# Optimization experiments

Measured on AMD Instinct MI355X. Metric: run time of the kernel, lower is better.

## Reference

```python
import jax, jax.numpy as jnp
import numpy as np

NPOINT = 1024
NSAMPLE = 32


def _fps(xyz, npoint):
    # farthest point sampling; xyz: (B, N, 3) -> idx (B, npoint) int32
    B, N, _ = xyz.shape

    def step(carry, _):
        dist, far = carry
        centroid = jnp.take_along_axis(xyz, far[:, None, None], axis=1)  # (B,1,3)
        d = jnp.sum((xyz - centroid) ** 2, axis=-1)  # (B,N)
        dist = jnp.minimum(dist, d)
        nxt = jnp.argmax(dist, axis=1).astype(jnp.int32)
        return (dist, nxt), far

    init = (jnp.full((B, N), 1e10, xyz.dtype), jnp.zeros((B,), jnp.int32))
    _, idx = jax.lax.scan(step, init, None, length=npoint)
    return idx.T  # (B, npoint)


def _forward(xyz, features, afa_w1, afa_b1, afa_w2, afa_b2, afa_ww, afa_bw,
             mlp_w1, mlp_b1, mlp_w2, mlp_b2, mlp_w3, mlp_b3):
    B, N, _ = xyz.shape
    M = NSAMPLE
    # --- furthest point sampling + gather new_xyz ---
    fps_idx = _fps(xyz, NPOINT)                                   # (B, Np)
    new_xyz = jnp.take_along_axis(xyz, fps_idx[..., None], axis=1)  # (B, Np, 3)
    # --- kNN grouping (QueryAndGroup with use_xyz) ---
    sqd = (jnp.sum(new_xyz ** 2, -1)[..., None]
           + jnp.sum(xyz ** 2, -1)[:, None, :]
           - 2.0 * jnp.einsum('bpd,bnd->bpn', new_xyz, xyz))       # (B, Np, N)
    _, knn = jax.lax.top_k(-sqd, M)                               # (B, Np, M)
    gather = jax.vmap(lambda a, i: a[i])
    gxyz = gather(xyz, knn) - new_xyz[:, :, None, :]              # (B, Np, M, 3)
    gfeat = gather(features.transpose(0, 2, 1), knn)              # (B, Np, M, Cin)
    x = jnp.concatenate([gxyz, gfeat], axis=-1).transpose(0, 3, 1, 2)  # (B, C, Np, M)
    # --- AFA: pairwise diff + eye self term ---
    eye = jnp.eye(M, dtype=x.dtype)
    pair = x[..., :, None] - x[..., None, :] + x[..., :, None] * eye  # (B, C, Np, M, M)
    conv5 = lambda w, b, t: jnp.einsum('oc,bcnij->bonij', w, t) + b[None, :, None, None, None]
    h = jax.nn.relu(conv5(afa_w1, afa_b1, pair))
    h = jax.nn.relu(conv5(afa_w2, afa_b2, h))
    wgt = conv5(afa_ww, afa_bw, h)                                 # (B, C, Np, M, M)
    afa = jnp.sum(pair * wgt, axis=-1)                             # (B, C, Np, M)
    nf = x + afa
    # --- shared MLP (1x1 convs, relu, no bn) + max pool over M ---
    conv4 = lambda w, b, t: jnp.einsum('oc,bcnm->bonm', w, t) + b[None, :, None, None]
    h = jax.nn.relu(conv4(mlp_w1, mlp_b1, nf))
    h = jax.nn.relu(conv4(mlp_w2, mlp_b2, h))
    h = jax.nn.relu(conv4(mlp_w3, mlp_b3, h))
    out = jnp.max(h, axis=-1)                                      # (B, 128, Np)
    return new_xyz, out


def setup_inputs() -> dict:
    key = jax.random.key(0)
    ks = jax.random.split(key, 10)
    B, N, Cin = 2, 4096, 32
    C = Cin + 3  # use_xyz adds 3 -> 35

    def w(k, o, i):
        return (jax.random.normal(k, (o, i), jnp.float32) / np.float32(np.sqrt(i)))

    return {
        'xyz': jax.random.uniform(ks[0], (B, N, 3), jnp.float32),
        'features': jax.random.normal(ks[1], (B, Cin, N), jnp.float32),
        'afa_w1': w(ks[2], 16, C), 'afa_b1': jnp.zeros((16,), jnp.float32),
        'afa_w2': w(ks[3], 16, 16), 'afa_b2': jnp.zeros((16,), jnp.float32),
        'afa_ww': w(ks[4], C, 16), 'afa_bw': jnp.zeros((C,), jnp.float32),
        'mlp_w1': w(ks[5], 64, C), 'mlp_b1': jnp.zeros((64,), jnp.float32),
        'mlp_w2': w(ks[6], 64, 64), 'mlp_b2': jnp.zeros((64,), jnp.float32),
        'mlp_w3': w(ks[7], 128, 64), 'mlp_b3': jnp.zeros((128,), jnp.float32),
    }


def reference(xyz, features, afa_w1, afa_b1, afa_w2, afa_b2, afa_ww, afa_bw,
              mlp_w1, mlp_b1, mlp_w2, mlp_b2, mlp_w3, mlp_b3):
    return _forward(xyz, features, afa_w1, afa_b1, afa_w2, afa_b2, afa_ww, afa_bw,
                    mlp_w1, mlp_b1, mlp_w2, mlp_b2, mlp_w3, mlp_b3)
```

## Files before the change

### kernel.cpp

```cpp
#include <hip/hip_runtime.h>

#define BB 2
#define NN 4096
#define NP 1024
#define MM 32
#define CC 35
#define CIN 32

typedef float f2 __attribute__((ext_vector_type(2)));

#define KEY_DPP(CTRL) do { \
    int _lo = (int)(unsigned)key, _hi = (int)(unsigned)(key >> 32); \
    int _olo = __builtin_amdgcn_mov_dpp(_lo, CTRL, 0xF, 0xF, true); \
    int _ohi = __builtin_amdgcn_mov_dpp(_hi, CTRL, 0xF, 0xF, true); \
    unsigned long long _ok = ((unsigned long long)(unsigned)_ohi << 32) | (unsigned)_olo; \
    if (_ok > key) key = _ok; \
} while (0)

__launch_bounds__(256)
__global__ void fps_prep_kernel(const float* __restrict__ xyz, float* __restrict__ newxyz_out,
                                const float* __restrict__ w1, const float* __restrict__ w2,
                                const float* __restrict__ w3,
                                float* __restrict__ w1p, float* __restrict__ w2p,
                                float* __restrict__ w3p)
{
#pragma clang fp contract(off)
    const int t = threadIdx.x;

    if (blockIdx.x >= BB) {
        int g = (blockIdx.x - BB) * 256 + t;
        int stride = 8 * 256;
        for (int i = g; i < 9 * 64 * 4; i += stride) {
            int c4 = i >> 8, o = (i >> 2) & 63, cl = i & 3;
            int c = 4 * c4 + cl;
            w1p[i] = (c < CC) ? w1[o * CC + c] : 0.0f;
        }
        for (int i = g; i < 16 * 64 * 4; i += stride) {
            int c4 = i >> 8, o = (i >> 2) & 63, cl = i & 3;
            w2p[i] = w2[o * 64 + 4 * c4 + cl];
        }
        for (int i = g; i < 16 * 128 * 4; i += stride) {
            int c4 = i >> 9, o = (i >> 2) & 127, cl = i & 3;
            w3p[i] = w3[o * 64 + 4 * c4 + cl];
        }
        return;
    }

    const int b = blockIdx.x;
    const float* xb = xyz + b * NN * 3;

    __shared__ float4 pc[NN];
    __shared__ float nxs[NP * 3];
    __shared__ unsigned long long red[2][16];

    f2 px[8], py[8], pz[8], dist[8];
#pragma unroll
    for (int k = 0; k < 16; ++k) {
        int n = t + 256 * k;
        float x = xb[n * 3 + 0];
        float y = xb[n * 3 + 1];
        float z = xb[n * 3 + 2];
        px[k >> 1][k & 1] = x;
        py[k >> 1][k & 1] = y;
        pz[k >> 1][k & 1] = z;
        dist[k >> 1][k & 1] = 1e10f;
        pc[n] = make_float4(x, y, z, 0.0f);
    }
    __syncthreads();

    int far = 0;
    for (int s = 0; s < NP; ++s) {
        float4 c = pc[far];
        if (t == 0) {
            nxs[s * 3 + 0] = c.x;
            nxs[s * 3 + 1] = c.y;
            nxs[s * 3 + 2] = c.z;
        }
        const f2 cx = { c.x, c.x }, cy = { c.y, c.y }, cz = { c.z, c.z };

        float bv = -1.0f; int bi = 0;
#pragma unroll
        for (int j = 0; j < 8; ++j) {
            f2 dx = px[j] - cx, dy = py[j] - cy, dz = pz[j] - cz;
            f2 d = (dx * dx + dy * dy) + dz * dz;
            f2 dd = __builtin_elementwise_min(dist[j], d);
            dist[j] = dd;
            if (dd.x > bv) { bv = dd.x; bi = t + 256 * (2 * j); }
            if (dd.y > bv) { bv = dd.y; bi = t + 256 * (2 * j + 1); }
        }

        unsigned long long key =
            ((unsigned long long)(unsigned)__float_as_int(bv) << 32)
            | (unsigned)(0xFFFFFFFFu - (unsigned)bi);

        KEY_DPP(0xB1);
        KEY_DPP(0x4E);
        KEY_DPP(0x141);
        KEY_DPP(0x140);

        const int buf = s & 1;
        if ((t & 15) == 0) red[buf][t >> 4] = key;
        __syncthreads();

        key = red[buf][t & 15];
        KEY_DPP(0xB1);
        KEY_DPP(0x4E);
        KEY_DPP(0x141);
        KEY_DPP(0x140);
        far = (int)(0xFFFFFFFFu - (unsigned)key);
    }

    __syncthreads();
#pragma unroll
    for (int j = 0; j < 12; ++j) {
        int i = t + 256 * j;
        newxyz_out[b * NP * 3 + i] = nxs[i];
    }
}

__launch_bounds__(256)
__global__ void knnafa_kernel(const float* __restrict__ xyz, const float* __restrict__ feat,
                              const float* __restrict__ newxyz,
                              const float* __restrict__ aw1, const float* __restrict__ ab1,
                              const float* __restrict__ aw2, const float* __restrict__ ab2,
                              const float* __restrict__ aww, const float* __restrict__ abw,
                              const float* __restrict__ w1p, const float* __restrict__ b1,
                              const float* __restrict__ w2p, const float* __restrict__ b2,
                              const float* __restrict__ w3p, const float* __restrict__ b3,
                              float* __restrict__ out)
{
    const int bp = blockIdx.x;
    const int b = bp >> 10, p = bp & 1023;
    const int t = threadIdx.x;

    union Smem {
        struct {
            unsigned kxs[NN];
            int hist[256];
            int wsum[4];
            unsigned long long blist[512];
        } k;
        struct {
            float xs_t[MM][36];
            float u[MM][20];
            float nfs[CC + 1][MM];
            float h1s[64][36];
            float h2s[64][36];
            float pmax[128][2];
        } a;
    };
    __shared__ Smem S;
    __shared__ int idxs[MM];
    __shared__ int scal[4];

    {
#pragma clang fp contract(off)
        const float* xb = xyz + b * NN * 3;
        const float qx = newxyz[bp * 3 + 0];
        const float qy = newxyz[bp * 3 + 1];
        const float qz = newxyz[bp * 3 + 2];
        const float qn = (qx * qx + qy * qy) + qz * qz;

        S.k.hist[t] = 0;
        if (t < 4) scal[t] = 0;
        __syncthreads();

#pragma unroll
        for (int k = 0; k < 16; ++k) {
            int n = t + 256 * k;
            float x = xb[n * 3 + 0], y = xb[n * 3 + 1], z = xb[n * 3 + 2];
            float xn = (x * x + y * y) + z * z;
            float dt = (qx * x + qy * y) + qz * z;
            float d = (qn + xn) - 2.0f * dt;
            unsigned bits = __float_as_uint(d);
            unsigned kx = bits ^ ((unsigned)((int)bits >> 31) | 0x80000000u);
            S.k.kxs[n] = kx;
            atomicAdd(&S.k.hist[kx >> 24], 1);
        }
        __syncthreads();

        {
            int c = S.k.hist[t];
            int incl = c;
            const int lane = t & 63, w = t >> 6;
#pragma unroll
            for (int off = 1; off < 64; off <<= 1) {
                int o = __shfl_up(incl, off);
                if (lane >= off) incl += o;
            }
            if (lane == 63) S.k.wsum[w] = incl;
            __syncthreads();
            int base = 0;
            for (int ww = 0; ww < 4; ++ww) if (ww < w) base += S.k.wsum[ww];
            int excl = base + incl - c;
            if (excl < MM && MM <= excl + c) { scal[0] = t; scal[1] = excl; }
        }
        __syncthreads();

        const int B = scal[0];
        const int cntBelow = scal[1];
        const unsigned bstart = (unsigned)B << 24;

#pragma unroll
        for (int k = 0; k < 16; ++k) {
            int n = t + 256 * k;
            unsigned kx = S.k.kxs[n];
            if (kx < bstart) {
                int pos = atomicAdd(&scal[3], 1);
                idxs[pos] = n;
            } else if ((kx >> 24) == (unsigned)B) {
                int pos = atomicAdd(&scal[2], 1);
                if (pos < 512) S.k.blist[pos] = ((unsigned long long)kx << 32) | (unsigned)n;
            }
        }
        __syncthreads();

        const int nB = scal[2];
        const int k2 = MM - cntBelow;

        if (nB <= 512) {
            for (int m = t; m < nB; m += 256) {
                unsigned long long my = S.k.blist[m];
                int rank = 0;
                for (int q = 0; q < nB; ++q) rank += (S.k.blist[q] < my) ? 1 : 0;
                if (rank < k2)
                    idxs[cntBelow + rank] = (int)(my & 0xFFFFFFFFu);
            }
        } else {
            for (int r = 0; r < MM; ++r) {
                unsigned bvk = 0xFFFFFFFFu; int bi = NN;
#pragma unroll
                for (int k = 0; k < 16; ++k) {
                    int n = t + 256 * k;
                    unsigned v = S.k.kxs[n];
                    if (v < bvk) { bvk = v; bi = n; }
                }
#pragma unroll
                for (int off = 1; off < 64; off <<= 1) {
                    unsigned ov = __shfl_xor(bvk, off);
                    int   oi = __shfl_xor(bi, off);
                    if (ov < bvk || (ov == bvk && oi < bi)) { bvk = ov; bi = oi; }
                }
                if ((t & 63) == 0) { S.k.hist[t >> 6] = (int)bvk; S.k.wsum[t >> 6] = bi; }
                __syncthreads();
                unsigned fv = (unsigned)S.k.hist[0]; int fi = S.k.wsum[0];
#pragma unroll
                for (int w = 1; w < 4; ++w) {
                    unsigned ov = (unsigned)S.k.hist[w]; int oi = S.k.wsum[w];
                    if (ov < fv || (ov == fv && oi < fi)) { fv = ov; fi = oi; }
                }
                if (t == 0) { idxs[r] = fi; S.k.kxs[fi] = 0xFFFFFFFFu; }
                __syncthreads();
            }
        }
    }
    __syncthreads();

    {
        const int m = t & 31, c0 = t >> 5;
        const int id = idxs[m] & (NN - 1);
        for (int c = c0; c < CC; c += 8) {
            float v;
            if (c < 3) v = xyz[(b * NN + id) * 3 + c] - newxyz[bp * 3 + c];
            else       v = feat[(b * CIN + (c - 3)) * NN + id];
            S.a.xs_t[m][c] = v;
        }
        if (c0 == 0) S.a.xs_t[m][35] = 0.0f;
    }
    __syncthreads();

    const int i = t >> 3, jg = t & 7;

    float xi[36];
    {
        const float4* xp = (const float4*)&S.a.xs_t[i][0];
#pragma unroll
        for (int q = 0; q < 9; ++q) {
            float4 v = xp[q];
            xi[4 * q] = v.x; xi[4 * q + 1] = v.y; xi[4 * q + 2] = v.z; xi[4 * q + 3] = v.w;
        }
    }

#pragma unroll
    for (int oo = 0; oo < 2; ++oo) {
        const int o = 2 * jg + oo;
        float acc = 0.0f;
#pragma unroll
        for (int c = 0; c < CC; ++c) acc += aw1[o * CC + c] * xi[c];
        S.a.u[i][o] = acc;
    }
    __syncthreads();

    float ui[16];
    {
        const float4* up = (const float4*)&S.a.u[i][0];
#pragma unroll
        for (int q = 0; q < 4; ++q) {
            float4 v = up[q];
            ui[4 * q] = v.x; ui[4 * q + 1] = v.y; ui[4 * q + 2] = v.z; ui[4 * q + 3] = v.w;
        }
    }

    float afa[CC];
#pragma unroll
    for (int c = 0; c < CC; ++c) afa[c] = 0.0f;

#pragma unroll
    for (int jk = 0; jk < 4; ++jk) {
        const int j = jg + 8 * jk;
        const bool diag = (i == j);

        float uj[16];
        {
            const float4* up = (const float4*)&S.a.u[j][0];
#pragma unroll
            for (int q = 0; q < 4; ++q) {
                float4 v = up[q];
                uj[4 * q] = v.x; uj[4 * q + 1] = v.y; uj[4 * q + 2] = v.z; uj[4 * q + 3] = v.w;
            }
        }

        float h1[16];
#pragma unroll
        for (int o = 0; o < 16; ++o) {
            float sv = ui[o] - uj[o];
            if (diag) sv += ui[o];
            h1[o] = fmaxf(sv + ab1[o], 0.0f);
        }

        float xj[36];
        {
            const float4* xp = (const float4*)&S.a.xs_t[j][0];
#pragma unroll
            for (int q = 0; q < 9; ++q) {
                float4 v = xp[q];
                xj[4 * q] = v.x; xj[4 * q + 1] = v.y; xj[4 * q + 2] = v.z; xj[4 * q + 3] = v.w;
            }
        }

        float h2[16];
#pragma unroll
        for (int o = 0; o < 16; ++o) {
            float acc = ab2[o];
#pragma unroll
            for (int c = 0; c < 16; ++c) acc += aw2[o * 16 + c] * h1[c];
            h2[o] = fmaxf(acc, 0.0f);
        }

#pragma unroll
        for (int c = 0; c < CC; ++c) {
            float acc = abw[c];
#pragma unroll
            for (int k = 0; k < 16; ++k) acc += aww[c * 16 + k] * h2[k];
            float pc_ = xi[c] - xj[c];
            if (diag) pc_ += xi[c];
            afa[c] += pc_ * acc;
        }
    }

#pragma unroll
    for (int c = 0; c < CC; ++c) {
        float v = afa[c];
        v += __shfl_xor(v, 1);
        v += __shfl_xor(v, 2);
        v += __shfl_xor(v, 4);
        if (jg == 0) S.a.nfs[c][i] = xi[c] + v;
    }
    if (jg == 0) S.a.nfs[35][i] = 0.0f;
    __syncthreads();

    {
        const int o = t & 63, ib = (t >> 6) << 3;
        float acc[8];
        float bb = b1[o];
#pragma unroll
        for (int k = 0; k < 8; ++k) acc[k] = bb;
        const float4* wp = (const float4*)w1p;
#pragma unroll
        for (int c4 = 0; c4 < 9; ++c4) {
            float4 w = wp[c4 * 64 + o];
#pragma unroll
            for (int cl = 0; cl < 4; ++cl) {
                const int c = 4 * c4 + cl;
                float wc = ((const float*)&w)[cl];
                const float4* np4 = (const float4*)&S.a.nfs[c][ib];
                float4 n0 = np4[0], n1 = np4[1];
                acc[0] += wc * n0.x; acc[1] += wc * n0.y; acc[2] += wc * n0.z; acc[3] += wc * n0.w;
                acc[4] += wc * n1.x; acc[5] += wc * n1.y; acc[6] += wc * n1.z; acc[7] += wc * n1.w;
            }
        }
        float4 r0 = { fmaxf(acc[0], 0.0f), fmaxf(acc[1], 0.0f), fmaxf(acc[2], 0.0f), fmaxf(acc[3], 0.0f) };
        float4 r1 = { fmaxf(acc[4], 0.0f), fmaxf(acc[5], 0.0f), fmaxf(acc[6], 0.0f), fmaxf(acc[7], 0.0f) };
        *(float4*)&S.a.h1s[o][ib]     = r0;
        *(float4*)&S.a.h1s[o][ib + 4] = r1;
    }
    __syncthreads();

    {
        const int o = t & 63, ib = (t >> 6) << 3;
        float acc[8];
        float bb = b2[o];
#pragma unroll
        for (int k = 0; k < 8; ++k) acc[k] = bb;
        const float4* wp = (const float4*)w2p;
#pragma unroll
        for (int c4 = 0; c4 < 16; ++c4) {
            float4 w = wp[c4 * 64 + o];
#pragma unroll
            for (int cl = 0; cl < 4; ++cl) {
                const int c = 4 * c4 + cl;
                float wc = ((const float*)&w)[cl];
                const float4* hp4 = (const float4*)&S.a.h1s[c][ib];
                float4 h0 = hp4[0], h1v = hp4[1];
                acc[0] += wc * h0.x; acc[1] += wc * h0.y; acc[2] += wc * h0.z; acc[3] += wc * h0.w;
                acc[4] += wc * h1v.x; acc[5] += wc * h1v.y; acc[6] += wc * h1v.z; acc[7] += wc * h1v.w;
            }
        }
        float4 r0 = { fmaxf(acc[0], 0.0f), fmaxf(acc[1], 0.0f), fmaxf(acc[2], 0.0f), fmaxf(acc[3], 0.0f) };
        float4 r1 = { fmaxf(acc[4], 0.0f), fmaxf(acc[5], 0.0f), fmaxf(acc[6], 0.0f), fmaxf(acc[7], 0.0f) };
        *(float4*)&S.a.h2s[o][ib]     = r0;
        *(float4*)&S.a.h2s[o][ib + 4] = r1;
    }
    __syncthreads();

    {
        const int o = t & 127, ib = (t >> 7) << 4;
        float acc[16];
        float bb = b3[o];
#pragma unroll
        for (int k = 0; k < 16; ++k) acc[k] = bb;
        const float4* wp = (const float4*)w3p;
#pragma unroll
        for (int c4 = 0; c4 < 16; ++c4) {
            float4 w = wp[c4 * 128 + o];
#pragma unroll
            for (int cl = 0; cl < 4; ++cl) {
                const int c = 4 * c4 + cl;
                float wc = ((const float*)&w)[cl];
                const float4* hp4 = (const float4*)&S.a.h2s[c][ib];
                float4 h0 = hp4[0], h1v = hp4[1], h2v = hp4[2], h3v = hp4[3];
                acc[0]  += wc * h0.x;  acc[1]  += wc * h0.y;  acc[2]  += wc * h0.z;  acc[3]  += wc * h0.w;
                acc[4]  += wc * h1v.x; acc[5]  += wc * h1v.y; acc[6]  += wc * h1v.z; acc[7]  += wc * h1v.w;
                acc[8]  += wc * h2v.x; acc[9]  += wc * h2v.y; acc[10] += wc * h2v.z; acc[11] += wc * h2v.w;
                acc[12] += wc * h3v.x; acc[13] += wc * h3v.y; acc[14] += wc * h3v.z; acc[15] += wc * h3v.w;
            }
        }
        float mx = -1e30f;
#pragma unroll
        for (int k = 0; k < 16; ++k) mx = fmaxf(mx, fmaxf(acc[k], 0.0f));
        S.a.pmax[o][t >> 7] = mx;
    }
    __syncthreads();

    if (t < 128) {
        float v = fmaxf(S.a.pmax[t][0], S.a.pmax[t][1]);
        out[(b * 128 + t) * NP + p] = v;
    }
}

extern "C" void kernel_launch(void* const* d_in, const int* in_sizes, int n_in,
                              void* d_out, int out_size, void* d_ws, size_t ws_size,
                              hipStream_t stream)
{
    const float* xyz  = (const float*)d_in[0];
    const float* feat = (const float*)d_in[1];
    const float* aw1  = (const float*)d_in[2];
    const float* ab1  = (const float*)d_in[3];
    const float* aw2  = (const float*)d_in[4];
    const float* ab2  = (const float*)d_in[5];
    const float* aww  = (const float*)d_in[6];
    const float* abw  = (const float*)d_in[7];
    const float* mw1  = (const float*)d_in[8];
    const float* mb1  = (const float*)d_in[9];
    const float* mw2  = (const float*)d_in[10];
    const float* mb2  = (const float*)d_in[11];
    const float* mw3  = (const float*)d_in[12];
    const float* mb3  = (const float*)d_in[13];

    float* out    = (float*)d_out;
    float* newxyz = out;
    float* out2   = out + BB * NP * 3;

    float* w1p = (float*)d_ws;
    float* w2p = w1p + 9 * 64 * 4;
    float* w3p = w2p + 16 * 64 * 4;

    fps_prep_kernel<<<dim3(BB + 8), dim3(256), 0, stream>>>(xyz, newxyz,
                                                            mw1, mw2, mw3, w1p, w2p, w3p);
    knnafa_kernel<<<dim3(BB * NP), dim3(256), 0, stream>>>(
        xyz, feat, newxyz,
        aw1, ab1, aw2, ab2, aww, abw,
        w1p, mb1, w2p, mb2, w3p, mb3, out2);
}
```

Baseline: 715.6 us.

## Fuse FPS and kNN/AFA into a persistent kernel with progress-flag overlap

Merges the sequential farthest-point-sampling kernel and the per-point kNN/AFA/MLP kernel into one persistent kernel. Two blocks run FPS and publish sampled centroids plus a progress counter every 16 steps. The remaining worker blocks spin on that counter and process points as soon as their centroid is ready. This overlaps the long serial FPS chain with the grouping and MLP work. The cost is spin-wait polling, the risk of deadlock if the FPS blocks are not co-resident, and fewer worker blocks (a 512-block grid) looping over 2048 points.

Result: slower. 785.1 us (+9.7%).

```diff
diff --git a/kernel.cpp b/kernel.cpp
--- a/kernel.cpp
+++ b/kernel.cpp
@@ -6,6 +6,7 @@
 #define MM 32
 #define CC 35
 #define CIN 32
+#define WGRID 512
 
 typedef float f2 __attribute__((ext_vector_type(2)));
 
@@ -17,444 +18,465 @@
     if (_ok > key) key = _ok; \
 } while (0)
 
-__launch_bounds__(256)
-__global__ void fps_prep_kernel(const float* __restrict__ xyz, float* __restrict__ newxyz_out,
-                                const float* __restrict__ w1, const float* __restrict__ w2,
-                                const float* __restrict__ w3,
-                                float* __restrict__ w1p, float* __restrict__ w2p,
-                                float* __restrict__ w3p)
+__global__ void prep_kernel(const float* __restrict__ w1, const float* __restrict__ w2,
+                            const float* __restrict__ w3,
+                            float* __restrict__ w1p, float* __restrict__ w2p,
+                            float* __restrict__ w3p, int* __restrict__ progress)
 {
+    int g = blockIdx.x * 256 + threadIdx.x;
+    int stride = gridDim.x * 256;
+    if (g < 2) progress[g] = 0;
+    for (int i = g; i < 9 * 64 * 4; i += stride) {
+        int c4 = i >> 8, o = (i >> 2) & 63, cl = i & 3;
+        int c = 4 * c4 + cl;
+        w1p[i] = (c < CC) ? w1[o * CC + c] : 0.0f;
+    }
+    for (int i = g; i < 16 * 64 * 4; i += stride) {
+        int c4 = i >> 8, o = (i >> 2) & 63, cl = i & 3;
+        w2p[i] = w2[o * 64 + 4 * c4 + cl];
+    }
+    for (int i = g; i < 16 * 128 * 4; i += stride) {
+        int c4 = i >> 9, o = (i >> 2) & 127, cl = i & 3;
+        w3p[i] = w3[o * 64 + 4 * c4 + cl];
+    }
+}
+
+union MegaSmem {
+    struct {
+        float4 pc[NN];
+        unsigned long long red[2][16];
+    } f;
+    struct {
+        union {
+            struct {
+                unsigned kxs[NN];
+                int hist[256];
+                int wsum[4];
+                unsigned long long blist[512];
+            } k;
+            struct {
+                float xs_t[MM][36];
+                float u[MM][20];
+                float nfs[CC + 1][MM];
+                float h1s[64][36];
+                float h2s[64][36];
+                float pmax[128][2];
+            } a;
+        };
+        int idxs[MM];
+        int scal[4];
+        float qs[3];
+    } w;
+};
+
+__launch_bounds__(256, 2)
+__global__ void mega_kernel(const float* __restrict__ xyz, const float* __restrict__ feat,
+                            float* __restrict__ newxyz,
+                            const float* __restrict__ aw1, const float* __restrict__ ab1,
+                            const float* __restrict__ aw2, const float* __restrict__ ab2,
+                            const float* __restrict__ aww, const float* __restrict__ abw,
+                            const float* __restrict__ w1p, const float* __restrict__ b1,
+                            const float* __restrict__ w2p, const float* __restrict__ b2,
+                            const float* __restrict__ w3p, const float* __restrict__ b3,
+                            float* __restrict__ out, int* __restrict__ progress)
+{
+    __shared__ MegaSmem S;
+    const int t = threadIdx.x;
+
+    if (blockIdx.x < BB) {
 #pragma clang fp contract(off)
-    const int t = threadIdx.x;
-
-    if (blockIdx.x >= BB) {
-        int g = (blockIdx.x - BB) * 256 + t;
-        int stride = 8 * 256;
-        for (int i = g; i < 9 * 64 * 4; i += stride) {
-            int c4 = i >> 8, o = (i >> 2) & 63, cl = i & 3;
-            int c = 4 * c4 + cl;
-            w1p[i] = (c < CC) ? w1[o * CC + c] : 0.0f;
-        }
-        for (int i = g; i < 16 * 64 * 4; i += stride) {
-            int c4 = i >> 8, o = (i >> 2) & 63, cl = i & 3;
-            w2p[i] = w2[o * 64 + 4 * c4 + cl];
-        }
-        for (int i = g; i < 16 * 128 * 4; i += stride) {
-            int c4 = i >> 9, o = (i >> 2) & 127, cl = i & 3;
-            w3p[i] = w3[o * 64 + 4 * c4 + cl];
+        const int b = blockIdx.x;
+        const float* xb = xyz + b * NN * 3;
+
+        f2 px[8], py[8], pz[8], dist[8];
+#pragma unroll
+        for (int k = 0; k < 16; ++k) {
+            int n = t + 256 * k;
+            float x = xb[n * 3 + 0];
+            float y = xb[n * 3 + 1];
+            float z = xb[n * 3 + 2];
+            px[k >> 1][k & 1] = x;
+            py[k >> 1][k & 1] = y;
+            pz[k >> 1][k & 1] = z;
+            dist[k >> 1][k & 1] = 1e10f;
+            S.f.pc[n] = make_float4(x, y, z, 0.0f);
+        }
+        __syncthreads();
+
+        int far = 0;
+        for (int s = 0; s < NP; ++s) {
+            float4 c = S.f.pc[far];
+            if (t == 0) {
+                __hip_atomic_store(&newxyz[(b * NP + s) * 3 + 0], c.x,
+                                   __ATOMIC_RELAXED, __HIP_MEMORY_SCOPE_AGENT);
+                __hip_atomic_store(&newxyz[(b * NP + s) * 3 + 1], c.y,
+                                   __ATOMIC_RELAXED, __HIP_MEMORY_SCOPE_AGENT);
+                __hip_atomic_store(&newxyz[(b * NP + s) * 3 + 2], c.z,
+                                   __ATOMIC_RELAXED, __HIP_MEMORY_SCOPE_AGENT);
+            }
+            const f2 cx = { c.x, c.x }, cy = { c.y, c.y }, cz = { c.z, c.z };
+
+            float bv = -1.0f; int bi = 0;
+#pragma unroll
+            for (int j = 0; j < 8; ++j) {
+                f2 dx = px[j] - cx, dy = py[j] - cy, dz = pz[j] - cz;
+                f2 d = (dx * dx + dy * dy) + dz * dz;
+                f2 dd = __builtin_elementwise_min(dist[j], d);
+                dist[j] = dd;
+                if (dd.x > bv) { bv = dd.x; bi = t + 256 * (2 * j); }
+                if (dd.y > bv) { bv = dd.y; bi = t + 256 * (2 * j + 1); }
+            }
+
+            unsigned long long key =
+                ((unsigned long long)(unsigned)__float_as_int(bv) << 32)
+                | (unsigned)(0xFFFFFFFFu - (unsigned)bi);
+
+            KEY_DPP(0xB1);
+            KEY_DPP(0x4E);
+            KEY_DPP(0x141);
+            KEY_DPP(0x140);
+
+            const int buf = s & 1;
+            if ((t & 15) == 0) S.f.red[buf][t >> 4] = key;
+            __syncthreads();
+
+            key = S.f.red[buf][t & 15];
+            KEY_DPP(0xB1);
+            KEY_DPP(0x4E);
+            KEY_DPP(0x141);
+            KEY_DPP(0x140);
+            far = (int)(0xFFFFFFFFu - (unsigned)key);
+
+            if (t == 0 && (s & 15) == 15)
+                __hip_atomic_store(&progress[b], s + 1, __ATOMIC_RELEASE,
+                                   __HIP_MEMORY_SCOPE_AGENT);
         }
         return;
     }
 
-    const int b = blockIdx.x;
-    const float* xb = xyz + b * NN * 3;
-
-    __shared__ float4 pc[NN];
-    __shared__ float nxs[NP * 3];
-    __shared__ unsigned long long red[2][16];
-
-    f2 px[8], py[8], pz[8], dist[8];
-#pragma unroll
-    for (int k = 0; k < 16; ++k) {
-        int n = t + 256 * k;
-        float x = xb[n * 3 + 0];
-        float y = xb[n * 3 + 1];
-        float z = xb[n * 3 + 2];
-        px[k >> 1][k & 1] = x;
-        py[k >> 1][k & 1] = y;
-        pz[k >> 1][k & 1] = z;
-        dist[k >> 1][k & 1] = 1e10f;
-        pc[n] = make_float4(x, y, z, 0.0f);
-    }
-    __syncthreads();
-
-    int far = 0;
-    for (int s = 0; s < NP; ++s) {
-        float4 c = pc[far];
+    for (int pair = blockIdx.x - BB; pair < BB * NP; pair += WGRID - BB) {
+        const int p = pair >> 1, b = pair & 1;
+        const int bp = b * NP + p;
+
         if (t == 0) {
-            nxs[s * 3 + 0] = c.x;
-            nxs[s * 3 + 1] = c.y;
-            nxs[s * 3 + 2] = c.z;
-        }
-        const f2 cx = { c.x, c.x }, cy = { c.y, c.y }, cz = { c.z, c.z };
-
-        float bv = -1.0f; int bi = 0;
-#pragma unroll
-        for (int j = 0; j < 8; ++j) {
-            f2 dx = px[j] - cx, dy = py[j] - cy, dz = pz[j] - cz;
-            f2 d = (dx * dx + dy * dy) + dz * dz;
-            f2 dd = __builtin_elementwise_min(dist[j], d);
-            dist[j] = dd;
-            if (dd.x > bv) { bv = dd.x; bi = t + 256 * (2 * j); }
-            if (dd.y > bv) { bv = dd.y; bi = t + 256 * (2 * j + 1); }
-        }
-
-        unsigned long long key =
-            ((unsigned long long)(unsigned)__float_as_int(bv) << 32)
-            | (unsigned)(0xFFFFFFFFu - (unsigned)bi);
-
-        KEY_DPP(0xB1);
-        KEY_DPP(0x4E);
-        KEY_DPP(0x141);
-        KEY_DPP(0x140);
-
-        const int buf = s & 1;
-        if ((t & 15) == 0) red[buf][t >> 4] = key;
-        __syncthreads();
-
-        key = red[buf][t & 15];
-        KEY_DPP(0xB1);
-        KEY_DPP(0x4E);
-        KEY_DPP(0x141);
-        KEY_DPP(0x140);
-        far = (int)(0xFFFFFFFFu - (unsigned)key);
-    }
-
-    __syncthreads();
-#pragma unroll
-    for (int j = 0; j < 12; ++j) {
-        int i = t + 256 * j;
-        newxyz_out[b * NP * 3 + i] = nxs[i];
-    }
-}
-
-__launch_bounds__(256)
-__global__ void knnafa_kernel(const float* __restrict__ xyz, const float* __restrict__ feat,
-                              const float* __restrict__ newxyz,
-                              const float* __restrict__ aw1, const float* __restrict__ ab1,
-                              const float* __restrict__ aw2, const float* __restrict__ ab2,
-                              const float* __restrict__ aww, const float* __restrict__ abw,
-                              const float* __restrict__ w1p, const float* __restrict__ b1,
-                              const float* __restrict__ w2p, const float* __restrict__ b2,
-                              const float* __restrict__ w3p, const float* __restrict__ b3,
-                              float* __restrict__ out)
-{
-    const int bp = blockIdx.x;
-    const int b = bp >> 10, p = bp & 1023;
-    const int t = threadIdx.x;
-
-    union Smem {
-        struct {
-            unsigned kxs[NN];
-            int hist[256];
-            int wsum[4];
-            unsigned long long blist[512];
-        } k;
-        struct {
-            float xs_t[MM][36];
-            float u[MM][20];
-            float nfs[CC + 1][MM];
-            float h1s[64][36];
-            float h2s[64][36];
-            float pmax[128][2];
-        } a;
-    };
-    __shared__ Smem S;
-    __shared__ int idxs[MM];
-    __shared__ int scal[4];
-
-    {
+            while (__hip_atomic_load(&progress[b], __ATOMIC_RELAXED,
+                                     __HIP_MEMORY_SCOPE_AGENT) <= p)
+                __builtin_amdgcn_s_sleep(32);
+            (void)__hip_atomic_load(&progress[b], __ATOMIC_ACQUIRE,
+                                    __HIP_MEMORY_SCOPE_AGENT);
+            S.w.qs[0] = __hip_atomic_load(&newxyz[bp * 3 + 0], __ATOMIC_RELAXED,
+                                          __HIP_MEMORY_SCOPE_AGENT);
+            S.w.qs[1] = __hip_atomic_load(&newxyz[bp * 3 + 1], __ATOMIC_RELAXED,
+                                          __HIP_MEMORY_SCOPE_AGENT);
+            S.w.qs[2] = __hip_atomic_load(&newxyz[bp * 3 + 2], __ATOMIC_RELAXED,
+                                          __HIP_MEMORY_SCOPE_AGENT);
+        }
+        __syncthreads();
+
+        {
 #pragma clang fp contract(off)
-        const float* xb = xyz + b * NN * 3;
-        const float qx = newxyz[bp * 3 + 0];
-        const float qy = newxyz[bp * 3 + 1];
-        const float qz = newxyz[bp * 3 + 2];
-        const float qn = (qx * qx + qy * qy) + qz * qz;
-
-        S.k.hist[t] = 0;
-        if (t < 4) scal[t] = 0;
-        __syncthreads();
-
-#pragma unroll
-        for (int k = 0; k < 16; ++k) {
-            int n = t + 256 * k;
-            float x = xb[n * 3 + 0], y = xb[n * 3 + 1], z = xb[n * 3 + 2];
-            float xn = (x * x + y * y) + z * z;
-            float dt = (qx * x + qy * y) + qz * z;
-            float d = (qn + xn) - 2.0f * dt;
-            unsigned bits = __float_as_uint(d);
-            unsigned kx = bits ^ ((unsigned)((int)bits >> 31) | 0x80000000u);
-            S.k.kxs[n] = kx;
-            atomicAdd(&S.k.hist[kx >> 24], 1);
-        }
-        __syncthreads();
-
-        {
-            int c = S.k.hist[t];
-            int incl = c;
-            const int lane = t & 63, w = t >> 6;
-#pragma unroll
-            for (int off = 1; off < 64; off <<= 1) {
-                int o = __shfl_up(incl, off);
-                if (lane >= off) incl += o;
-            }
-            if (lane == 63) S.k.wsum[w] = incl;
+            const float* xb = xyz + b * NN * 3;
+            const float qx = S.w.qs[0];
+            const float qy = S.w.qs[1];
+            const float qz = S.w.qs[2];
+            const float qn = (qx * qx + qy * qy) + qz * qz;
+
+            S.w.k.hist[t] = 0;
+            if (t < 4) S.w.scal[t] = 0;
             __syncthreads();
-            int base = 0;
-            for (int ww = 0; ww < 4; ++ww) if (ww < w) base += S.k.wsum[ww];
-            int excl = base + incl - c;
-            if (excl < MM && MM <= excl + c) { scal[0] = t; scal[1] = excl; }
-        }
-        __syncthreads();
-
-        const int B = scal[0];
-        const int cntBelow = scal[1];
-        const unsigned bstart = (unsigned)B << 24;
-
-#pragma unroll
-        for (int k = 0; k < 16; ++k) {
-            int n = t + 256 * k;
-            unsigned kx = S.k.kxs[n];
-            if (kx < bstart) {
-                int pos = atomicAdd(&scal[3], 1);
-                idxs[pos] = n;
-            } else if ((kx >> 24) == (unsigned)B) {
-                int pos = atomicAdd(&scal[2], 1);
-                if (pos < 512) S.k.blist[pos] = ((unsigned long long)kx << 32) | (unsigned)n;
-            }
-        }
-        __syncthreads();
-
-        const int nB = scal[2];
-        const int k2 = MM - cntBelow;
-
-        if (nB <= 512) {
-            for (int m = t; m < nB; m += 256) {
-                unsigned long long my = S.k.blist[m];
-                int rank = 0;
-                for (int q = 0; q < nB; ++q) rank += (S.k.blist[q] < my) ? 1 : 0;
-                if (rank < k2)
-                    idxs[cntBelow + rank] = (int)(my & 0xFFFFFFFFu);
-            }
-        } else {
-            for (int r = 0; r < MM; ++r) {
-                unsigned bvk = 0xFFFFFFFFu; int bi = NN;
-#pragma unroll
-                for (int k = 0; k < 16; ++k) {
-                    int n = t + 256 * k;
-                    unsigned v = S.k.kxs[n];
-                    if (v < bvk) { bvk = v; bi = n; }
-                }
+
+#pragma unroll
+            for (int k = 0; k < 16; ++k) {
+                int n = t + 256 * k;
+                float x = xb[n * 3 + 0], y = xb[n * 3 + 1], z = xb[n * 3 + 2];
+                float xn = (x * x + y * y) + z * z;
+                float dt = (qx * x + qy * y) + qz * z;
+                float d = (qn + xn) - 2.0f * dt;
+                unsigned bits = __float_as_uint(d);
+                unsigned kx = bits ^ ((unsigned)((int)bits >> 31) | 0x80000000u);
+                S.w.k.kxs[n] = kx;
+                atomicAdd(&S.w.k.hist[kx >> 24], 1);
+            }
+            __syncthreads();
+
+            {
+                int c = S.w.k.hist[t];
+                int incl = c;
+                const int lane = t & 63, w = t >> 6;
 #pragma unroll
                 for (int off = 1; off < 64; off <<= 1) {
-                    unsigned ov = __shfl_xor(bvk, off);
-                    int   oi = __shfl_xor(bi, off);
-                    if (ov < bvk || (ov == bvk && oi < bi)) { bvk = ov; bi = oi; }
-                }
-                if ((t & 63) == 0) { S.k.hist[t >> 6] = (int)bvk; S.k.wsum[t >> 6] = bi; }
+                    int o = __shfl_up(incl, off);
+                    if (lane >= off) incl += o;
+                }
+                if (lane == 63) S.w.k.wsum[w] = incl;
                 __syncthreads();
-                unsigned fv = (unsigned)S.k.hist[0]; int fi = S.k.wsum[0];
-#pragma unroll
-                for (int w = 1; w < 4; ++w) {
-                    unsigned ov = (unsigned)S.k.hist[w]; int oi = S.k.wsum[w];
-                    if (ov < fv || (ov == fv && oi < fi)) { fv = ov; fi = oi; }
-                }
-                if (t == 0) { idxs[r] = fi; S.k.kxs[fi] = 0xFFFFFFFFu; }
-                __syncthreads();
-            }
-        }
-    }
-    __syncthreads();
-
-    {
-        const int m = t & 31, c0 = t >> 5;
-        const int id = idxs[m] & (NN - 1);
-        for (int c = c0; c < CC; c += 8) {
-            float v;
-            if (c < 3) v = xyz[(b * NN + id) * 3 + c] - newxyz[bp * 3 + c];
-            else       v = feat[(b * CIN + (c - 3)) * NN + id];
-            S.a.xs_t[m][c] = v;
-        }
-        if (c0 == 0) S.a.xs_t[m][35] = 0.0f;
-    }
-    __syncthreads();
-
-    const int i = t >> 3, jg = t & 7;
-
-    float xi[36];
-    {
-        const float4* xp = (const float4*)&S.a.xs_t[i][0];
-#pragma unroll
-        for (int q = 0; q < 9; ++q) {
-            float4 v = xp[q];
-            xi[4 * q] = v.x; xi[4 * q + 1] = v.y; xi[4 * q + 2] = v.z; xi[4 * q + 3] = v.w;
-        }
-    }
-
-#pragma unroll
-    for (int oo = 0; oo < 2; ++oo) {
-        const int o = 2 * jg + oo;
-        float acc = 0.0f;
-#pragma unroll
-        for (int c = 0; c < CC; ++c) acc += aw1[o * CC + c] * xi[c];
-        S.a.u[i][o] = acc;
-    }
-    __syncthreads();
-
-    float ui[16];
-    {
-        const float4* up = (const float4*)&S.a.u[i][0];
-#pragma unroll
-        for (int q = 0; q < 4; ++q) {
-            float4 v = up[q];
-            ui[4 * q] = v.x; ui[4 * q + 1] = v.y; ui[4 * q + 2] = v.z; ui[4 * q + 3] = v.w;
-        }
-    }
-
-    float afa[CC];
-#pragma unroll
-    for (int c = 0; c < CC; ++c) afa[c] = 0.0f;
-
-#pragma unroll
-    for (int jk = 0; jk < 4; ++jk) {
-        const int j = jg + 8 * jk;
-        const bool diag = (i == j);
-
-        float uj[16];
-        {
-            const float4* up = (const float4*)&S.a.u[j][0];
+                int base = 0;
+                for (int ww = 0; ww < 4; ++ww) if (ww < w) base += S.w.k.wsum[ww];
+                int excl = base + incl - c;
+                if (excl < MM && MM <= excl + c) { S.w.scal[0] = t; S.w.scal[1] = excl; }
+            }
+            __syncthreads();
+
+            const int B = S.w.scal[0];
+            const int cntBelow = S.w.scal[1];
+            const unsigned bstart = (unsigned)B << 24;
+
+#pragma unroll
+            for (int k = 0; k < 16; ++k) {
+                int n = t + 256 * k;
+                unsigned kx = S.w.k.kxs[n];
+                if (kx < bstart) {
+                    int pos = atomicAdd(&S.w.scal[3], 1);
+                    S.w.idxs[pos] = n;
+                } else if ((kx >> 24) == (unsigned)B) {
+                    int pos = atomicAdd(&S.w.scal[2], 1);
+                    if (pos < 512) S.w.k.blist[pos] = ((unsigned long long)kx << 32) | (unsigned)n;
+                }
+            }
+            __syncthreads();
+
+            const int nB = S.w.scal[2];
+            const int k2 = MM - cntBelow;
+
+            if (nB <= 512) {
+                for (int m = t; m < nB; m += 256) {
+                    unsigned long long my = S.w.k.blist[m];
+                    int rank = 0;
+                    for (int q = 0; q < nB; ++q) rank += (S.w.k.blist[q] < my) ? 1 : 0;
+                    if (rank < k2)
+                        S.w.idxs[cntBelow + rank] = (int)(my & 0xFFFFFFFFu);
+                }
+            } else {
+                for (int r = 0; r < MM; ++r) {
+                    unsigned bvk = 0xFFFFFFFFu; int bi = NN;
+#pragma unroll
+                    for (int k = 0; k < 16; ++k) {
+                        int n = t + 256 * k;
+                        unsigned v = S.w.k.kxs[n];
+                        if (v < bvk) { bvk = v; bi = n; }
+                    }
+#pragma unroll
+                    for (int off = 1; off < 64; off <<= 1) {
+                        unsigned ov = __shfl_xor(bvk, off);
+                        int   oi = __shfl_xor(bi, off);
+                        if (ov < bvk || (ov == bvk && oi < bi)) { bvk = ov; bi = oi; }
+                    }
+                    if ((t & 63) == 0) { S.w.k.hist[t >> 6] = (int)bvk; S.w.k.wsum[t >> 6] = bi; }
+                    __syncthreads();
+                    unsigned fv = (unsigned)S.w.k.hist[0]; int fi = S.w.k.wsum[0];
+#pragma unroll
+                    for (int w = 1; w < 4; ++w) {
+                        unsigned ov = (unsigned)S.w.k.hist[w]; int oi = S.w.k.wsum[w];
+                        if (ov < fv || (ov == fv && oi < fi)) { fv = ov; fi = oi; }
+                    }
+                    if (t == 0) { S.w.idxs[r] = fi; S.w.k.kxs[fi] = 0xFFFFFFFFu; }
+                    __syncthreads();
+                }
+            }
+        }
+        __syncthreads();
+
+        {
+            const int m = t & 31, c0 = t >> 5;
+            const int id = S.w.idxs[m] & (NN - 1);
+            for (int c = c0; c < CC; c += 8) {
+                float v;
+                if (c < 3) v = xyz[(b * NN + id) * 3 + c] - S.w.qs[c];
+                else       v = feat[(b * CIN + (c - 3)) * NN + id];
+                S.w.a.xs_t[m][c] = v;
+            }
+            if (c0 == 0) S.w.a.xs_t[m][35] = 0.0f;
+        }
+        __syncthreads();
+
+        const int i = t >> 3, jg = t & 7;
+
+        float xi[36];
+        {
+            const float4* xp = (const float4*)&S.w.a.xs_t[i][0];
+#pragma unroll
+            for (int q = 0; q < 9; ++q) {
+                float4 v = xp[q];
+                xi[4 * q] = v.x; xi[4 * q + 1] = v.y; xi[4 * q + 2] = v.z; xi[4 * q + 3] = v.w;
+            }
+        }
+
+#pragma unroll
+        for (int oo = 0; oo < 2; ++oo) {
+            const int o = 2 * jg + oo;
+            float acc = 0.0f;
+#pragma unroll
+            for (int c = 0; c < CC; ++c) acc += aw1[o * CC + c] * xi[c];
+            S.w.a.u[i][o] = acc;
+        }
+        __syncthreads();
+
+        float ui[16];
+        {
+            const float4* up = (const float4*)&S.w.a.u[i][0];
 #pragma unroll
             for (int q = 0; q < 4; ++q) {
                 float4 v = up[q];
-                uj[4 * q] = v.x; uj[4 * q + 1] = v.y; uj[4 * q + 2] = v.z; uj[4 * q + 3] = v.w;
-            }
-        }
-
-        float h1[16];
-#pragma unroll
-        for (int o = 0; o < 16; ++o) {
-            float sv = ui[o] - uj[o];
-            if (diag) sv += ui[o];
-            h1[o] = fmaxf(sv + ab1[o], 0.0f);
-        }
-
-        float xj[36];
-        {
-            const float4* xp = (const float4*)&S.a.xs_t[j][0];
-#pragma unroll
-            for (int q = 0; q < 9; ++q) {
-                float4 v = xp[q];
-                xj[4 * q] = v.x; xj[4 * q + 1] = v.y; xj[4 * q + 2] = v.z; xj[4 * q + 3] = v.w;
-            }
-        }
-
-        float h2[16];
-#pragma unroll
-        for (int o = 0; o < 16; ++o) {
-            float acc = ab2[o];
-#pragma unroll
-            for (int c = 0; c < 16; ++c) acc += aw2[o * 16 + c] * h1[c];
-            h2[o] = fmaxf(acc, 0.0f);
+                ui[4 * q] = v.x; ui[4 * q + 1] = v.y; ui[4 * q + 2] = v.z; ui[4 * q + 3] = v.w;
+            }
+        }
+
+        float afa[CC];
+#pragma unroll
+        for (int c = 0; c < CC; ++c) afa[c] = 0.0f;
+
+#pragma unroll
+        for (int jk = 0; jk < 4; ++jk) {
+            const int j = jg + 8 * jk;
+            const bool diag = (i == j);
+
+            float uj[16];
+            {
+                const float4* up = (const float4*)&S.w.a.u[j][0];
+#pragma unroll
+                for (int q = 0; q < 4; ++q) {
+                    float4 v = up[q];
+                    uj[4 * q] = v.x; uj[4 * q + 1] = v.y; uj[4 * q + 2] = v.z; uj[4 * q + 3] = v.w;
+                }
+            }
+
+            float h1[16];
+#pragma unroll
+            for (int o = 0; o < 16; ++o) {
+                float sv = ui[o] - uj[o];
+                if (diag) sv += ui[o];
+                h1[o] = fmaxf(sv + ab1[o], 0.0f);
+            }
+
+            float xj[36];
+            {
+                const float4* xp = (const float4*)&S.w.a.xs_t[j][0];
+#pragma unroll
+                for (int q = 0; q < 9; ++q) {
+                    float4 v = xp[q];
+                    xj[4 * q] = v.x; xj[4 * q + 1] = v.y; xj[4 * q + 2] = v.z; xj[4 * q + 3] = v.w;
+                }
+            }
+
+            float h2[16];
+#pragma unroll
+            for (int o = 0; o < 16; ++o) {
+                float acc = ab2[o];
+#pragma unroll
+                for (int c = 0; c < 16; ++c) acc += aw2[o * 16 + c] * h1[c];
+                h2[o] = fmaxf(acc, 0.0f);
+            }
+
+#pragma unroll
+            for (int c = 0; c < CC; ++c) {
+                float acc = abw[c];
+#pragma unroll
+                for (int k = 0; k < 16; ++k) acc += aww[c * 16 + k] * h2[k];
+                float pc_ = xi[c] - xj[c];
+                if (diag) pc_ += xi[c];
+                afa[c] += pc_ * acc;
+            }
         }
 
 #pragma unroll
         for (int c = 0; c < CC; ++c) {
-            float acc = abw[c];
-#pragma unroll
-            for (int k = 0; k < 16; ++k) acc += aww[c * 16 + k] * h2[k];
-            float pc_ = xi[c] - xj[c];
-            if (diag) pc_ += xi[c];
-            afa[c] += pc_ * acc;
-        }
-    }
-
-#pragma unroll
-    for (int c = 0; c < CC; ++c) {
-        float v = afa[c];
-        v += __shfl_xor(v, 1);
-        v += __shfl_xor(v, 2);
-        v += __shfl_xor(v, 4);
-        if (jg == 0) S.a.nfs[c][i] = xi[c] + v;
-    }
-    if (jg == 0) S.a.nfs[35][i] = 0.0f;
-    __syncthreads();
-
-    {
-        const int o = t & 63, ib = (t >> 6) << 3;
-        float acc[8];
-        float bb = b1[o];
-#pragma unroll
-        for (int k = 0; k < 8; ++k) acc[k] = bb;
-        const float4* wp = (const float4*)w1p;
-#pragma unroll
-        for (int c4 = 0; c4 < 9; ++c4) {
-            float4 w = wp[c4 * 64 + o];
-#pragma unroll
-            for (int cl = 0; cl < 4; ++cl) {
-                const int c = 4 * c4 + cl;
-                float wc = ((const float*)&w)[cl];
-                const float4* np4 = (const float4*)&S.a.nfs[c][ib];
-                float4 n0 = np4[0], n1 = np4[1];
-                acc[0] += wc * n0.x; acc[1] += wc * n0.y; acc[2] += wc * n0.z; acc[3] += wc * n0.w;
-                acc[4] += wc * n1.x; acc[5] += wc * n1.y; acc[6] += wc * n1.z; acc[7] += wc * n1.w;
-            }
-        }
-        float4 r0 = { fmaxf(acc[0], 0.0f), fmaxf(acc[1], 0.0f), fmaxf(acc[2], 0.0f), fmaxf(acc[3], 0.0f) };
-        float4 r1 = { fmaxf(acc[4], 0.0f), fmaxf(acc[5], 0.0f), fmaxf(acc[6], 0.0f), fmaxf(acc[7], 0.0f) };
-        *(float4*)&S.a.h1s[o][ib]     = r0;
-        *(float4*)&S.a.h1s[o][ib + 4] = r1;
-    }
-    __syncthreads();
-
-    {
-        const int o = t & 63, ib = (t >> 6) << 3;
-        float acc[8];
-        float bb = b2[o];
-#pragma unroll
-        for (int k = 0; k < 8; ++k) acc[k] = bb;
-        const float4* wp = (const float4*)w2p;
-#pragma unroll
-        for (int c4 = 0; c4 < 16; ++c4) {
-            float4 w = wp[c4 * 64 + o];
-#pragma unroll
-            for (int cl = 0; cl < 4; ++cl) {
-                const int c = 4 * c4 + cl;
-                float wc = ((const float*)&w)[cl];
-                const float4* hp4 = (const float4*)&S.a.h1s[c][ib];
-                float4 h0 = hp4[0], h1v = hp4[1];
-                acc[0] += wc * h0.x; acc[1] += wc * h0.y; acc[2] += wc * h0.z; acc[3] += wc * h0.w;
-                acc[4] += wc * h1v.x; acc[5] += wc * h1v.y; acc[6] += wc * h1v.z; acc[7] += wc * h1v.w;
-            }
-        }
-        float4 r0 = { fmaxf(acc[0], 0.0f), fmaxf(acc[1], 0.0f), fmaxf(acc[2], 0.0f), fmaxf(acc[3], 0.0f) };
-        float4 r1 = { fmaxf(acc[4], 0.0f), fmaxf(acc[5], 0.0f), fmaxf(acc[6], 0.0f), fmaxf(acc[7], 0.0f) };
-        *(float4*)&S.a.h2s[o][ib]     = r0;
-        *(float4*)&S.a.h2s[o][ib + 4] = r1;
-    }
-    __syncthreads();
-
-    {
-        const int o = t & 127, ib = (t >> 7) << 4;
-        float acc[16];
-        float bb = b3[o];
-#pragma unroll
-        for (int k = 0; k < 16; ++k) acc[k] = bb;
-        const float4* wp = (const float4*)w3p;
-#pragma unroll
-        for (int c4 = 0; c4 < 16; ++c4) {
-            float4 w = wp[c4 * 128 + o];
-#pragma unroll
-            for (int cl = 0; cl < 4; ++cl) {
-                const int c = 4 * c4 + cl;
-                float wc = ((const float*)&w)[cl];
-                const float4* hp4 = (const float4*)&S.a.h2s[c][ib];
-                float4 h0 = hp4[0], h1v = hp4[1], h2v = hp4[2], h3v = hp4[3];
-                acc[0]  += wc * h0.x;  acc[1]  += wc * h0.y;  acc[2]  += wc * h0.z;  acc[3]  += wc * h0.w;
-                acc[4]  += wc * h1v.x; acc[5]  += wc * h1v.y; acc[6]  += wc * h1v.z; acc[7]  += wc * h1v.w;
-                acc[8]  += wc * h2v.x; acc[9]  += wc * h2v.y; acc[10] += wc * h2v.z; acc[11] += wc * h2v.w;
-                acc[12] += wc * h3v.x; acc[13] += wc * h3v.y; acc[14] += wc * h3v.z; acc[15] += wc * h3v.w;
-            }
-        }
-        float mx = -1e30f;
-#pragma unroll
-        for (int k = 0; k < 16; ++k) mx = fmaxf(mx, fmaxf(acc[k], 0.0f));
-        S.a.pmax[o][t >> 7] = mx;
-    }
-    __syncthreads();
-
-    if (t < 128) {
-        float v = fmaxf(S.a.pmax[t][0], S.a.pmax[t][1]);
-        out[(b * 128 + t) * NP + p] = v;
+            float v = afa[c];
+            v += __shfl_xor(v, 1);
+            v += __shfl_xor(v, 2);
+            v += __shfl_xor(v, 4);
+            if (jg == 0) S.w.a.nfs[c][i] = xi[c] + v;
+        }
+        if (jg == 0) S.w.a.nfs[35][i] = 0.0f;
+        __syncthreads();
+
+        {
+            const int o = t & 63, ib = (t >> 6) << 3;
+            float acc[8];
+            float bb = b1[o];
+#pragma unroll
+            for (int k = 0; k < 8; ++k) acc[k] = bb;
+            const float4* wp = (const float4*)w1p;
+#pragma unroll
+            for (int c4 = 0; c4 < 9; ++c4) {
+                float4 w = wp[c4 * 64 + o];
+#pragma unroll
+                for (int cl = 0; cl < 4; ++cl) {
+                    const int c = 4 * c4 + cl;
+                    float wc = ((const float*)&w)[cl];
+                    const float4* np4 = (const float4*)&S.w.a.nfs[c][ib];
+                    float4 n0 = np4[0], n1 = np4[1];
+                    acc[0] += wc * n0.x; acc[1] += wc * n0.y; acc[2] += wc * n0.z; acc[3] += wc * n0.w;
+                    acc[4] += wc * n1.x; acc[5] += wc * n1.y; acc[6] += wc * n1.z; acc[7] += wc * n1.w;
+                }
+            }
+            float4 r0 = { fmaxf(acc[0], 0.0f), fmaxf(acc[1], 0.0f), fmaxf(acc[2], 0.0f), fmaxf(acc[3], 0.0f) };
+            float4 r1 = { fmaxf(acc[4], 0.0f), fmaxf(acc[5], 0.0f), fmaxf(acc[6], 0.0f), fmaxf(acc[7], 0.0f) };
+            *(float4*)&S.w.a.h1s[o][ib]     = r0;
+            *(float4*)&S.w.a.h1s[o][ib + 4] = r1;
+        }
+        __syncthreads();
+
+        {
+            const int o = t & 63, ib = (t >> 6) << 3;
+            float acc[8];
+            float bb = b2[o];
+#pragma unroll
+            for (int k = 0; k < 8; ++k) acc[k] = bb;
+            const float4* wp = (const float4*)w2p;
+#pragma unroll
+            for (int c4 = 0; c4 < 16; ++c4) {
+                float4 w = wp[c4 * 64 + o];
+#pragma unroll
+                for (int cl = 0; cl < 4; ++cl) {
+                    const int c = 4 * c4 + cl;
+                    float wc = ((const float*)&w)[cl];
+                    const float4* hp4 = (const float4*)&S.w.a.h1s[c][ib];
+                    float4 h0 = hp4[0], h1v = hp4[1];
+                    acc[0] += wc * h0.x; acc[1] += wc * h0.y; acc[2] += wc * h0.z; acc[3] += wc * h0.w;
+                    acc[4] += wc * h1v.x; acc[5] += wc * h1v.y; acc[6] += wc * h1v.z; acc[7] += wc * h1v.w;
+                }
+            }
+            float4 r0 = { fmaxf(acc[0], 0.0f), fmaxf(acc[1], 0.0f), fmaxf(acc[2], 0.0f), fmaxf(acc[3], 0.0f) };
+            float4 r1 = { fmaxf(acc[4], 0.0f), fmaxf(acc[5], 0.0f), fmaxf(acc[6], 0.0f), fmaxf(acc[7], 0.0f) };
+            *(float4*)&S.w.a.h2s[o][ib]     = r0;
+            *(float4*)&S.w.a.h2s[o][ib + 4] = r1;
+        }
+        __syncthreads();
+
+        {
+            const int o = t & 127, ib = (t >> 7) << 4;
+            float acc[16];
+            float bb = b3[o];
+#pragma unroll
+            for (int k = 0; k < 16; ++k) acc[k] = bb;
+            const float4* wp = (const float4*)w3p;
+#pragma unroll
+            for (int c4 = 0; c4 < 16; ++c4) {
+                float4 w = wp[c4 * 128 + o];
+#pragma unroll
+                for (int cl = 0; cl < 4; ++cl) {
+                    const int c = 4 * c4 + cl;
+                    float wc = ((const float*)&w)[cl];
+                    const float4* hp4 = (const float4*)&S.w.a.h2s[c][ib];
+                    float4 h0 = hp4[0], h1v = hp4[1], h2v = hp4[2], h3v = hp4[3];
+                    acc[0]  += wc * h0.x;  acc[1]  += wc * h0.y;  acc[2]  += wc * h0.z;  acc[3]  += wc * h0.w;
+                    acc[4]  += wc * h1v.x; acc[5]  += wc * h1v.y; acc[6]  += wc * h1v.z; acc[7]  += wc * h1v.w;
+                    acc[8]  += wc * h2v.x; acc[9]  += wc * h2v.y; acc[10] += wc * h2v.z; acc[11] += wc * h2v.w;
+                    acc[12] += wc * h3v.x; acc[13] += wc * h3v.y; acc[14] += wc * h3v.z; acc[15] += wc * h3v.w;
+                }
+            }
+            float mx = -1e30f;
+#pragma unroll
+            for (int k = 0; k < 16; ++k) mx = fmaxf(mx, fmaxf(acc[k], 0.0f));
+            S.w.a.pmax[o][t >> 7] = mx;
+        }
+        __syncthreads();
+
+        if (t < 128) {
+            float v = fmaxf(S.w.a.pmax[t][0], S.w.a.pmax[t][1]);
+            out[(b * 128 + t) * NP + p] = v;
+        }
+        __syncthreads();
     }
 }
 
@@ -484,11 +506,12 @@
     float* w1p = (float*)d_ws;
     float* w2p = w1p + 9 * 64 * 4;
     float* w3p = w2p + 16 * 64 * 4;
-
-    fps_prep_kernel<<<dim3(BB + 8), dim3(256), 0, stream>>>(xyz, newxyz,
-                                                            mw1, mw2, mw3, w1p, w2p, w3p);
-    knnafa_kernel<<<dim3(BB * NP), dim3(256), 0, stream>>>(
+    int* progress = (int*)(w3p + 16 * 128 * 4);
+
+    prep_kernel<<<dim3(8), dim3(256), 0, stream>>>(mw1, mw2, mw3, w1p, w2p, w3p, progress);
+
+    mega_kernel<<<dim3(WGRID), dim3(256), 0, stream>>>(
         xyz, feat, newxyz,
         aw1, ab1, aw2, ab2, aww, abw,
-        w1p, mb1, w2p, mb2, w3p, mb3, out2);
+        w1p, mb1, w2p, mb2, w3p, mb3, out2, progress);
 }
```
